# Performance work log

Measured on AMD Instinct MI355X. Metric: run time of the kernel, lower is better.

The kernel has to match this reference:

```python
import jax, jax.numpy as jnp
import numpy as np

B = 4096
V = 50257
K = 64
LABEL_SMOOTHING = 0.1


def setup_inputs() -> dict:
    key = jax.random.key(0)
    k1, k2 = jax.random.split(key)
    inp = jax.random.normal(k1, (B, V), dtype=jnp.float32)
    target = jax.random.randint(k2, (B,), 0, V, dtype=jnp.int64)
    return {"input": inp, "target": target}


def reference(input, target):
    rows = jnp.arange(input.shape[0])
    # gather the true-class logit: (B, 1)
    truth = input[rows, target][:, None]
    # mask the true class to -inf so top-k selects k hardest negatives
    masked = input.at[rows, target].set(-jnp.inf)
    topk_vals = jax.lax.top_k(masked, K)[0]          # (B, K)
    selected = jnp.concatenate([truth, topk_vals], axis=-1)  # (B, K+1)
    # cross-entropy with target class 0 and label smoothing (torch semantics:
    # loss = (1-eps)*nll + eps * mean_c(-log p_c))
    logp = jax.nn.log_softmax(selected, axis=-1)
    nll = -logp[:, 0]
    smooth = -jnp.mean(logp, axis=-1)
    per_ex = (1.0 - LABEL_SMOOTHING) * nll + LABEL_SMOOTHING * smooth
    return jnp.mean(per_ex)
```

## Files before the change

### kernel.cpp

```cpp
#include <hip/hip_runtime.h>
#include <math.h>
#include <stdint.h>

#define BROWS 4096
#define VCOLS 50257
#define KTOP  64
#define CAP   2048
#define CHECK_AT 1024
#define NREG 32

__device__ __forceinline__ unsigned f2key(float f) {
    unsigned u = __float_as_uint(f);
    return u ^ ((unsigned)((int)u >> 31) | 0x80000000u);
}
__device__ __forceinline__ float key2f(unsigned k) {
    unsigned u = (k & 0x80000000u) ? (k ^ 0x80000000u) : ~k;
    return __uint_as_float(u);
}

__device__ __forceinline__ int wave_sum_i(int c) {
    #pragma unroll
    for (int d = 1; d < 64; d <<= 1) c += __shfl_xor(c, d);
    return c;
}

__device__ __forceinline__ void load_keys(const float* s_buf, unsigned cnt, int lane, unsigned* key) {
    #pragma unroll
    for (int j = 0; j < NREG / 4; ++j) {
        const float4 v = ((const float4*)s_buf)[j * 64 + lane];
        const int base = (j * 64 + lane) * 4;
        key[4*j+0] = (base + 0 < (int)cnt) ? f2key(v.x) : 0u;
        key[4*j+1] = (base + 1 < (int)cnt) ? f2key(v.y) : 0u;
        key[4*j+2] = (base + 2 < (int)cnt) ? f2key(v.z) : 0u;
        key[4*j+3] = (base + 3 < (int)cnt) ? f2key(v.w) : 0u;
    }
}

__device__ __attribute__((noinline)) unsigned long long
wave_compact_f(float* s_buf, unsigned cnt, unsigned lo_in, int lane) {
    __builtin_amdgcn_wave_barrier();
    unsigned key[NREG];
    load_keys(s_buf, cnt, lane, key);
    unsigned kmx = 0u;
    #pragma unroll
    for (int j = 0; j < NREG; ++j) kmx = max(kmx, key[j]);
    #pragma unroll
    for (int d = 1; d < 64; d <<= 1) kmx = max(kmx, (unsigned)__shfl_xor((int)kmx, d));

    unsigned lo = lo_in;
    unsigned hi = kmx + 1u;
    for (int it = 0; it < 12; ++it) {
        if (hi - lo <= 1u) break;
        const unsigned mid = lo + ((hi - lo) >> 1);
        int c = 0;
        #pragma unroll
        for (int j = 0; j < NREG; ++j) c += (key[j] >= mid) ? 1 : 0;
        c = wave_sum_i(c);
        if (c >= KTOP) lo = mid; else hi = mid;
    }
    int cl = 0; unsigned sm = 0u;
    #pragma unroll
    for (int j = 0; j < NREG; ++j) { const bool s = key[j] >= lo; sm |= (unsigned)s << j; cl += s ? 1 : 0; }
    int incl = cl;
    #pragma unroll
    for (int d = 1; d < 64; d <<= 1) { const int t = __shfl_up(incl, d); if (lane >= d) incl += t; }
    int pos = incl - cl;
    __builtin_amdgcn_wave_barrier();
    #pragma unroll
    for (int j = 0; j < NREG; ++j) if ((sm >> j) & 1u) s_buf[pos++] = key2f(key[j]);
    const unsigned ncnt = (unsigned)__shfl(incl, 63);
    __builtin_amdgcn_wave_barrier();
    return ((unsigned long long)ncnt << 32) | (unsigned long long)lo;
}

__device__ __forceinline__ float wave_final(const float* s_buf, unsigned cnt, float thr, float tv, int lane) {
    __builtin_amdgcn_wave_barrier();
    unsigned key[NREG];
    load_keys(s_buf, cnt, lane, key);
    unsigned kmx = 0u;
    #pragma unroll
    for (int j = 0; j < NREG; ++j) kmx = max(kmx, key[j]);
    #pragma unroll
    for (int d = 1; d < 64; d <<= 1) kmx = max(kmx, (unsigned)__shfl_xor((int)kmx, d));

    unsigned lo = f2key(thr);
    unsigned hi = kmx + 1u;
    while (hi - lo > 1u) {
        const unsigned mid = lo + ((hi - lo) >> 1);
        int c = 0;
        #pragma unroll
        for (int j = 0; j < NREG; ++j) c += (key[j] >= mid) ? 1 : 0;
        c = wave_sum_i(c);
        if (c >= KTOP) lo = mid; else hi = mid;
    }
    const float vmax = key2f(kmx);
    const float m = fmaxf(vmax, tv);
    float se = 0.f, sv = 0.f; int cg = 0;
    #pragma unroll
    for (int j = 0; j < NREG; ++j) {
        if (key[j] > lo) { const float v = key2f(key[j]); se += __expf(v - m); sv += v; ++cg; }
    }
    #pragma unroll
    for (int d = 1; d < 64; d <<= 1) {
        se += __shfl_xor(se, d); sv += __shfl_xor(sv, d); cg += __shfl_xor(cg, d);
    }
    const float v64 = key2f(lo);
    const int nb = KTOP - cg;
    se += (float)nb * __expf(v64 - m);
    sv += (float)nb * v64;
    se += __expf(tv - m);
    const float lse = m + __logf(se);
    return lse - 0.9f * tv - 0.1f * ((sv + tv) * (1.0f / 65.0f));
}

__device__ __forceinline__ void ins1(float v, int gi, int tgt, float thr,
                                     float* s_buf, unsigned& cnt, unsigned long long lt) {
    const bool p = (v > thr) && (gi != tgt);
    const unsigned long long mk = __ballot(p ? 1 : 0);
    if (mk) {
        if (p) {
            const unsigned pos = cnt + (unsigned)__popcll(mk & lt);
            if (pos < CAP) s_buf[pos] = v;
        }
        cnt += (unsigned)__popcll(mk);
    }
}
__device__ __forceinline__ void ins4(const float4 q, int gb, int tgt, float thr,
                                     float* s_buf, unsigned& cnt, unsigned long long lt) {
    ins1(q.x, gb + 0, tgt, thr, s_buf, cnt, lt);
    ins1(q.y, gb + 1, tgt, thr, s_buf, cnt, lt);
    ins1(q.z, gb + 2, tgt, thr, s_buf, cnt, lt);
    ins1(q.w, gb + 3, tgt, thr, s_buf, cnt, lt);
}

__global__ __launch_bounds__(64) void topk_ce_kernel(
        const float* __restrict__ input, const int* __restrict__ target,
        float* __restrict__ per_ex, float* __restrict__ out_atomic) {
    __shared__ float s_buf[CAP];
    const int row  = blockIdx.x;
    const int lane = threadIdx.x;
    const float* __restrict__ rowp = input + (size_t)row * (size_t)VCOLS;
    const int tgt = target[row];
    const float tv = rowp[tgt];
    const unsigned long long lt = (1ull << lane) - 1ull;

    unsigned cnt = 0u;
    float thr = -INFINITY;

    const int pad = (int)((4u - ((((uintptr_t)rowp) >> 2) & 3u)) & 3u);
    {
        const float v = (lane < pad) ? rowp[lane] : 0.f;
        const bool p = (lane < pad) && (lane != tgt);
        const unsigned long long mk = __ballot(p ? 1 : 0);
        if (p) s_buf[cnt + __popcll(mk & lt)] = v;
        cnt += (unsigned)__popcll(mk);
    }

    const int nvec  = (VCOLS - pad) >> 2;
    const int ntail = (VCOLS - pad) & 3;
    const float4* __restrict__ vp = (const float4*)(rowp + pad);
    const int ntf = nvec >> 11;

    for (int t = 0; t < ntf; ++t) {
        const int b = (t << 11) + lane;
        float4 v[32];
        #pragma unroll
        for (int j = 0; j < 32; ++j) v[j] = vp[b + j * 64];
        #pragma unroll
        for (int c = 0; c < 8; ++c) {
            const float m0 = fmaxf(fmaxf(v[4*c+0].x, v[4*c+0].y), fmaxf(v[4*c+0].z, v[4*c+0].w));
            const float m1 = fmaxf(fmaxf(v[4*c+1].x, v[4*c+1].y), fmaxf(v[4*c+1].z, v[4*c+1].w));
            const float m2 = fmaxf(fmaxf(v[4*c+2].x, v[4*c+2].y), fmaxf(v[4*c+2].z, v[4*c+2].w));
            const float m3 = fmaxf(fmaxf(v[4*c+3].x, v[4*c+3].y), fmaxf(v[4*c+3].z, v[4*c+3].w));
            const float mh = fmaxf(fmaxf(m0, m1), fmaxf(m2, m3));
            if (__ballot((mh > thr) ? 1 : 0)) {
                ins4(v[4*c+0], pad + 4 * (b + (4*c+0) * 64), tgt, thr, s_buf, cnt, lt);
                ins4(v[4*c+1], pad + 4 * (b + (4*c+1) * 64), tgt, thr, s_buf, cnt, lt);
                ins4(v[4*c+2], pad + 4 * (b + (4*c+2) * 64), tgt, thr, s_buf, cnt, lt);
                ins4(v[4*c+3], pad + 4 * (b + (4*c+3) * 64), tgt, thr, s_buf, cnt, lt);
            }
            if (cnt > CHECK_AT) {
                const unsigned long long r = wave_compact_f(s_buf, cnt, f2key(thr), lane);
                cnt = (unsigned)(r >> 32); thr = key2f((unsigned)r);
            }
        }
    }

    for (int k0 = ntf << 11; k0 < nvec; k0 += 64) {
        const int idx = k0 + lane;
        float4 a;
        if (idx < nvec) a = vp[idx];
        else { a.x = a.y = a.z = a.w = -INFINITY; }
        const float mA = fmaxf(fmaxf(a.x, a.y), fmaxf(a.z, a.w));
        if (__ballot((mA > thr) ? 1 : 0)) ins4(a, pad + 4 * idx, tgt, thr, s_buf, cnt, lt);
        if (cnt > CHECK_AT) {
            const unsigned long long r = wave_compact_f(s_buf, cnt, f2key(thr), lane);
            cnt = (unsigned)(r >> 32); thr = key2f((unsigned)r);
        }
    }

    {
        const int idx = pad + 4 * nvec + lane;
        const float v = (lane < ntail) ? rowp[idx] : 0.f;
        const bool p = (lane < ntail) && (v > thr) && (idx != tgt);
        const unsigned long long mk = __ballot(p ? 1 : 0);
        if (p) {
            const unsigned pos = cnt + (unsigned)__popcll(mk & lt);
            if (pos < CAP) s_buf[pos] = v;
        }
        cnt += (unsigned)__popcll(mk);
    }

    const float pe = wave_final(s_buf, cnt, thr, tv, lane);
    if (lane == 0) {
        if (per_ex) per_ex[row] = pe;
        else atomicAdd(out_atomic, pe * (1.0f / BROWS));
    }
}

__global__ __launch_bounds__(256) void reduce_mean_kernel(
        const float* __restrict__ per_ex, float* __restrict__ out) {
    __shared__ float s[256];
    const int tid = threadIdx.x;
    const float4* p4 = (const float4*)per_ex;
    float acc = 0.0f;
    #pragma unroll
    for (int i = 0; i < BROWS / 1024; ++i) {
        const float4 v = p4[i * 256 + tid];
        acc += (v.x + v.y) + (v.z + v.w);
    }
    s[tid] = acc;
    __syncthreads();
    for (int w = 128; w > 0; w >>= 1) {
        if (tid < w) s[tid] += s[tid + w];
        __syncthreads();
    }
    if (tid == 0) out[0] = s[0] * (1.0f / BROWS);
}

extern "C" void kernel_launch(void* const* d_in, const int* in_sizes, int n_in,
                              void* d_out, int out_size, void* d_ws, size_t ws_size,
                              hipStream_t stream) {
    const float* input  = (const float*)d_in[0];
    const int*   target = (const int*)d_in[1];
    float* out = (float*)d_out;

    if (ws_size >= BROWS * sizeof(float)) {
        float* per_ex = (float*)d_ws;
        topk_ce_kernel<<<BROWS, 64, 0, stream>>>(input, target, per_ex, nullptr);
        reduce_mean_kernel<<<1, 256, 0, stream>>>(per_ex, out);
    } else {
        hipMemsetAsync(d_out, 0, sizeof(float), stream);
        topk_ce_kernel<<<BROWS, 64, 0, stream>>>(input, target, nullptr, out);
    }
}
```

Measured before the change: 212.8 us.

## Replace batched row loads with 8-stage register ring prefetch

The per-wave row scan used to load 32 float4s per lane in one batch and then process them. It now keeps an 8-slot register ring of 4 float4s per slot and issues the load for chunk t+8 while chunk t is being filtered, so memory latency overlaps with compute continuously. The compaction routine is also changed from noinline to forceinline and updates cnt/thr by reference. Inlining compaction together with the ring may raise register pressure and code size, which could reduce occupancy.

```diff
diff --git a/kernel.cpp b/kernel.cpp
--- a/kernel.cpp
+++ b/kernel.cpp
@@ -36,8 +36,7 @@
     }
 }
 
-__device__ __attribute__((noinline)) unsigned long long
-wave_compact_f(float* s_buf, unsigned cnt, unsigned lo_in, int lane) {
+__device__ __forceinline__ void wave_compact(float* s_buf, unsigned& cnt, float& thr, int lane) {
     __builtin_amdgcn_wave_barrier();
     unsigned key[NREG];
     load_keys(s_buf, cnt, lane, key);
@@ -47,7 +46,7 @@
     #pragma unroll
     for (int d = 1; d < 64; d <<= 1) kmx = max(kmx, (unsigned)__shfl_xor((int)kmx, d));
 
-    unsigned lo = lo_in;
+    unsigned lo = f2key(thr);
     unsigned hi = kmx + 1u;
     for (int it = 0; it < 12; ++it) {
         if (hi - lo <= 1u) break;
@@ -68,9 +67,9 @@
     __builtin_amdgcn_wave_barrier();
     #pragma unroll
     for (int j = 0; j < NREG; ++j) if ((sm >> j) & 1u) s_buf[pos++] = key2f(key[j]);
-    const unsigned ncnt = (unsigned)__shfl(incl, 63);
-    __builtin_amdgcn_wave_barrier();
-    return ((unsigned long long)ncnt << 32) | (unsigned long long)lo;
+    cnt = (unsigned)__shfl(incl, 63);
+    thr = key2f(lo);
+    __builtin_amdgcn_wave_barrier();
 }
 
 __device__ __forceinline__ float wave_final(const float* s_buf, unsigned cnt, float thr, float tv, int lane) {
@@ -159,44 +158,61 @@
     const int nvec  = (VCOLS - pad) >> 2;
     const int ntail = (VCOLS - pad) & 3;
     const float4* __restrict__ vp = (const float4*)(rowp + pad);
-    const int ntf = nvec >> 11;
-
-    for (int t = 0; t < ntf; ++t) {
-        const int b = (t << 11) + lane;
-        float4 v[32];
+    const int ntf = nvec >> 8;
+
+    float4 ring[8][4];
+    #pragma unroll
+    for (int s = 0; s < 8; ++s) {
+        if (s < ntf) {
+            const int b = s * 256 + lane;
+            ring[s][0] = vp[b];
+            ring[s][1] = vp[b + 64];
+            ring[s][2] = vp[b + 128];
+            ring[s][3] = vp[b + 192];
+        }
+    }
+
+    for (int t = 0; t < ntf; t += 8) {
         #pragma unroll
-        for (int j = 0; j < 32; ++j) v[j] = vp[b + j * 64];
-        #pragma unroll
-        for (int c = 0; c < 8; ++c) {
-            const float m0 = fmaxf(fmaxf(v[4*c+0].x, v[4*c+0].y), fmaxf(v[4*c+0].z, v[4*c+0].w));
-            const float m1 = fmaxf(fmaxf(v[4*c+1].x, v[4*c+1].y), fmaxf(v[4*c+1].z, v[4*c+1].w));
-            const float m2 = fmaxf(fmaxf(v[4*c+2].x, v[4*c+2].y), fmaxf(v[4*c+2].z, v[4*c+2].w));
-            const float m3 = fmaxf(fmaxf(v[4*c+3].x, v[4*c+3].y), fmaxf(v[4*c+3].z, v[4*c+3].w));
-            const float mh = fmaxf(fmaxf(m0, m1), fmaxf(m2, m3));
-            if (__ballot((mh > thr) ? 1 : 0)) {
-                ins4(v[4*c+0], pad + 4 * (b + (4*c+0) * 64), tgt, thr, s_buf, cnt, lt);
-                ins4(v[4*c+1], pad + 4 * (b + (4*c+1) * 64), tgt, thr, s_buf, cnt, lt);
-                ins4(v[4*c+2], pad + 4 * (b + (4*c+2) * 64), tgt, thr, s_buf, cnt, lt);
-                ins4(v[4*c+3], pad + 4 * (b + (4*c+3) * 64), tgt, thr, s_buf, cnt, lt);
+        for (int s = 0; s < 8; ++s) {
+            const int tq = t + s;
+            if (tq < ntf) {
+                const int bq = tq * 256 + lane;
+                const float4 q0 = ring[s][0];
+                const float4 q1 = ring[s][1];
+                const float4 q2 = ring[s][2];
+                const float4 q3 = ring[s][3];
+                if (tq + 8 < ntf) {
+                    const int bn = (tq + 8) * 256 + lane;
+                    ring[s][0] = vp[bn];
+                    ring[s][1] = vp[bn + 64];
+                    ring[s][2] = vp[bn + 128];
+                    ring[s][3] = vp[bn + 192];
+                }
+                const float m0 = fmaxf(fmaxf(q0.x, q0.y), fmaxf(q0.z, q0.w));
+                const float m1 = fmaxf(fmaxf(q1.x, q1.y), fmaxf(q1.z, q1.w));
+                const float m2 = fmaxf(fmaxf(q2.x, q2.y), fmaxf(q2.z, q2.w));
+                const float m3 = fmaxf(fmaxf(q3.x, q3.y), fmaxf(q3.z, q3.w));
+                const float m16 = fmaxf(fmaxf(m0, m1), fmaxf(m2, m3));
+                if (__ballot((m16 > thr) ? 1 : 0)) {
+                    ins4(q0, pad + 4 * bq,         tgt, thr, s_buf, cnt, lt);
+                    ins4(q1, pad + 4 * (bq + 64),  tgt, thr, s_buf, cnt, lt);
+                    ins4(q2, pad + 4 * (bq + 128), tgt, thr, s_buf, cnt, lt);
+                    ins4(q3, pad + 4 * (bq + 192), tgt, thr, s_buf, cnt, lt);
+                }
+                if (cnt > CHECK_AT) wave_compact(s_buf, cnt, thr, lane);
             }
-            if (cnt > CHECK_AT) {
-                const unsigned long long r = wave_compact_f(s_buf, cnt, f2key(thr), lane);
-                cnt = (unsigned)(r >> 32); thr = key2f((unsigned)r);
-            }
-        }
-    }
-
-    for (int k0 = ntf << 11; k0 < nvec; k0 += 64) {
+        }
+    }
+
+    for (int k0 = ntf << 8; k0 < nvec; k0 += 64) {
         const int idx = k0 + lane;
         float4 a;
         if (idx < nvec) a = vp[idx];
         else { a.x = a.y = a.z = a.w = -INFINITY; }
         const float mA = fmaxf(fmaxf(a.x, a.y), fmaxf(a.z, a.w));
         if (__ballot((mA > thr) ? 1 : 0)) ins4(a, pad + 4 * idx, tgt, thr, s_buf, cnt, lt);
-        if (cnt > CHECK_AT) {
-            const unsigned long long r = wave_compact_f(s_buf, cnt, f2key(thr), lane);
-            cnt = (unsigned)(r >> 32); thr = key2f((unsigned)r);
-        }
+        if (cnt > CHECK_AT) wave_compact(s_buf, cnt, thr, lane);
     }
 
     {
```

Result: slower. 217.8 us (+2.3%).
